# Optimization experiments

Hardware: AMD Instinct MI355X
Metric: run time of the kernel (lower is better)

The kernel has to match this reference:

```python
import jax, jax.numpy as jnp
import numpy as np
from jax import lax

B, L, D = 2, 2048, 128
H, HD = 8, 32
WIN = 3

def setup_inputs() -> dict:
    key = jax.random.key(0)
    ks = jax.random.split(key, 7)
    s = 0.05
    return {
        "x":  jax.random.normal(ks[0], (B, L, D), jnp.float32),
        "pe": jax.random.normal(ks[1], (L, D), jnp.float32) * s,
        "Wq": jax.random.normal(ks[2], (D, H * HD), jnp.float32) * s,
        "bq": jnp.zeros((H * HD,), jnp.float32),
        "Wk": jax.random.normal(ks[3], (D, H * HD), jnp.float32) * s,
        "bk": jnp.zeros((H * HD,), jnp.float32),
        "Wv": jax.random.normal(ks[4], (D, H), jnp.float32) * s,
    }

def reference(x, pe, Wq, bq, Wk, bk, Wv):
    b, l, d = x.shape
    h = Wv.shape[1]
    hd = Wq.shape[1] // h
    xp = x + pe                                   # (B,L,D)
    # split heads: Dense output columns [i*hd:(i+1)*hd] -> head i
    q = (xp @ Wq + bq).reshape(b, l, h, hd).transpose(2, 0, 1, 3)  # (H,B,L,hd)
    k = (xp @ Wk + bk).reshape(b, l, h, hd).transpose(2, 0, 1, 3)  # (H,B,L,hd)
    v = jax.nn.sigmoid(x @ Wv).transpose(2, 0, 1)                  # (H,B,L)

    attn = jnp.einsum('hbqd,hbkd->hbqk', q, k) * (float(hd) ** -0.5)
    attn = jax.nn.softmax(attn, axis=-1)          # (H,B,L,L)

    # band_part(0,-1) + diag_part(k=(0,L-1)) (RIGHT_LEFT align) + transpose + reverse(-2,-1)
    # collapses to the skew-gather: R[p, m] = attn[L-1-p-m, L-1-p] for p+m <= L-1 else 0
    p = jnp.arange(l)[:, None]                    # (L,1)
    m = jnp.arange(l)[None, :]                    # (1,L)
    ii = l - 1 - p - m                            # row index  (L,L)
    jj = jnp.broadcast_to(l - 1 - p, (l, l))      # col index  (L,L)
    valid = (ii >= 0)
    R = attn[:, :, jnp.where(valid, ii, 0), jj] * valid.astype(attn.dtype)  # (H,B,L,L)

    R = R * v[:, :, :, None]                      # gate by value, broadcast over distance axis

    # TF avg_pool excludes padding from the divisor
    sums = lax.reduce_window(R, 0.0, lax.add, (1, 1, 1, WIN), (1, 1, 1, 1), 'SAME')
    cnt = lax.reduce_window(jnp.ones((l,), R.dtype), 0.0, lax.add, (WIN,), (1,), 'SAME')
    pooled = sums / cnt                           # (H,B,L,L)

    # global mode: sum over position axis, -> (B, L_dist, H)
    out = pooled.sum(axis=2).transpose(1, 2, 0)
    return out
```

## Files before the change

kernel.cpp:

```cpp
#include <hip/hip_runtime.h>
#include <hip/hip_bf16.h>

#define LSEQ 2048
#define BB 2
#define DD 128
#define HH 8
#define HD 32

#define FPSCALE 524288.0f
#define RFPSCALE (1.0f / 524288.0f)
#define QSCALE 0.25503486f

typedef __bf16 bf8_t __attribute__((ext_vector_type(8)));
typedef __bf16 bf4_t __attribute__((ext_vector_type(4)));
typedef float f4_t __attribute__((ext_vector_type(4)));

static __device__ __forceinline__ float fexp2(float x) {
#if __has_builtin(__builtin_amdgcn_exp2f)
    return __builtin_amdgcn_exp2f(x);
#else
    float r;
    asm("v_exp_f32 %0, %1" : "=v"(r) : "v"(x));
    return r;
#endif
}

__global__ __launch_bounds__(256) void k_A(const float* __restrict__ x,
                                           const float* __restrict__ pe,
                                           const float* __restrict__ Wq,
                                           const float* __restrict__ Wk,
                                           const float* __restrict__ Wv,
                                           const float* __restrict__ bq,
                                           const float* __restrict__ bk,
                                           float* __restrict__ w,
                                           __bf16* __restrict__ Qb,
                                           __bf16* __restrict__ Kb,
                                           int* __restrict__ Si) {
    __shared__ __align__(16) char smem[34816];
    int gb = blockIdx.x;
    int tid = threadIdx.x;

    if (gb < 512) {
        __bf16* xs = (__bf16*)smem;
        __bf16* Wt = (__bf16*)(smem + 64 * 136 * 2);
        int jr = gb >> 3, y = gb & 7;
        int row0 = jr * 64;
        bool isK = y >= 4;
        int cbase = (y & 3) * 64;
        const float* W = isK ? Wk : Wq;

        #pragma unroll
        for (int i = 0; i < 8; i++) {
            int idx4 = tid + i * 256;
            int row = idx4 >> 5, col4 = idx4 & 31;
            float4 xv = ((const float4*)x)[row0 * 32 + idx4];
            float4 pv = ((const float4*)pe)[((row0 + row) & (LSEQ - 1)) * 32 + col4];
            bf4_t o = {(__bf16)(xv.x + pv.x), (__bf16)(xv.y + pv.y),
                       (__bf16)(xv.z + pv.z), (__bf16)(xv.w + pv.w)};
            *(bf4_t*)&xs[row * 136 + col4 * 4] = o;
        }
        #pragma unroll
        for (int i = 0; i < 8; i++) {
            int idx4 = tid + i * 256;
            int d = idx4 >> 4, c4 = (idx4 & 15) * 4;
            float4 wv4 = *(const float4*)(W + d * 256 + cbase + c4);
            Wt[(c4 + 0) * 136 + d] = (__bf16)wv4.x;
            Wt[(c4 + 1) * 136 + d] = (__bf16)wv4.y;
            Wt[(c4 + 2) * 136 + d] = (__bf16)wv4.z;
            Wt[(c4 + 3) * 136 + d] = (__bf16)wv4.w;
        }
        __syncthreads();

        int wid = tid >> 6, lane = tid & 63;
        int lm = lane & 15, lq = lane >> 4;
        int c0loc = wid * 16;
        f4_t acc0 = {0,0,0,0}, acc1 = {0,0,0,0}, acc2 = {0,0,0,0}, acc3 = {0,0,0,0};
        #pragma unroll
        for (int s = 0; s < 4; s++) {
            bf8_t bw = *(const bf8_t*)&Wt[(c0loc + lm) * 136 + lq * 8 + s * 32];
            bf8_t a0 = *(const bf8_t*)&xs[(0  + lm) * 136 + lq * 8 + s * 32];
            bf8_t a1 = *(const bf8_t*)&xs[(16 + lm) * 136 + lq * 8 + s * 32];
            bf8_t a2 = *(const bf8_t*)&xs[(32 + lm) * 136 + lq * 8 + s * 32];
            bf8_t a3 = *(const bf8_t*)&xs[(48 + lm) * 136 + lq * 8 + s * 32];
            acc0 = __builtin_amdgcn_mfma_f32_16x16x32_bf16(a0, bw, acc0, 0, 0, 0);
            acc1 = __builtin_amdgcn_mfma_f32_16x16x32_bf16(a1, bw, acc1, 0, 0, 0);
            acc2 = __builtin_amdgcn_mfma_f32_16x16x32_bf16(a2, bw, acc2, 0, 0, 0);
            acc3 = __builtin_amdgcn_mfma_f32_16x16x32_bf16(a3, bw, acc3, 0, 0, 0);
        }
        int c = cbase + c0loc + lm;
        float bv = (isK ? bk : bq)[c];
        float qs = isK ? 1.f : QSCALE;
        __bf16* Out = isK ? Kb : Qb;
        int h = c >> 5, hd = c & 31;
        f4_t accs[4] = {acc0, acc1, acc2, acc3};
        #pragma unroll
        for (int rs = 0; rs < 4; rs++) {
            #pragma unroll
            for (int r = 0; r < 4; r++) {
                int row = row0 + rs * 16 + lq * 4 + r;
                int b_ = row >> 11, l = row & (LSEQ - 1);
                Out[((h * BB + b_) * LSEQ + l) * HD + hd] =
                    (__bf16)((accs[rs][r] + bv) * qs);
            }
        }
    } else if (gb < 640) {
        float* xsf = (float*)smem;
        float* wvf = (float*)(smem + 32 * 132 * 4);
        int r0 = (gb - 512) * 32;
        for (int i = 0; i < 16; i++) {
            int idx = tid + i * 256;
            xsf[(idx >> 7) * 132 + (idx & 127)] = x[r0 * 128 + idx];
        }
        for (int i = 0; i < 4; i++) {
            int idx = tid + i * 256;
            wvf[idx] = Wv[idx];
        }
        __syncthreads();
        int rl = tid >> 3, h = tid & 7;
        float acc = 0.f;
        #pragma unroll 8
        for (int d = 0; d < 128; d++) acc += xsf[rl * 132 + d] * wvf[d * 8 + h];
        float sg = 1.f / (1.f + __expf(-acc));
        int r = r0 + rl;
        int b = r >> 11, l = r & (LSEQ - 1);
        w[(h * BB + b) * LSEQ + (LSEQ - 1 - l)] = sg * FPSCALE;
    } else {
        int4 z = {0, 0, 0, 0};
        ((int4*)Si)[(gb - 640) * 256 + tid] = z;
    }
}

__global__ __launch_bounds__(256) void k_F(const __bf16* __restrict__ Qb,
                                           const __bf16* __restrict__ Kb,
                                           const float* __restrict__ w,
                                           int* __restrict__ S) {
    __shared__ int Sloc[2048];
    __shared__ float dred[64];
    __shared__ float rdv_s[16];

    int hb = blockIdx.y;
    int q0 = blockIdx.x << 4;
    int tid = threadIdx.x;
    int wid = tid >> 6, lane = tid & 63;
    int lm = lane & 15, lq = lane >> 4;

    int4 z4 = {0, 0, 0, 0};
    ((int4*)Sloc)[tid] = z4;
    ((int4*)Sloc)[tid + 256] = z4;

    const __bf16* Qhb = Qb + hb * LSEQ * HD;
    const __bf16* Khb = Kb + hb * LSEQ * HD;
    bf8_t aq = *(const bf8_t*)(Qhb + (q0 + lm) * HD + lq * 8);

    float dsum[4] = {0.f, 0.f, 0.f, 0.f};
    #pragma unroll 4
    for (int s = wid; s < 128; s += 4) {
        bf8_t bk_ = *(const bf8_t*)(Khb + (s * 16 + lm) * HD + lq * 8);
        f4_t z = {0.f, 0.f, 0.f, 0.f};
        f4_t sc = __builtin_amdgcn_mfma_f32_16x16x32_bf16(aq, bk_, z, 0, 0, 0);
        #pragma unroll
        for (int r = 0; r < 4; r++) dsum[r] += fexp2(sc[r]);
    }
    #pragma unroll
    for (int r = 0; r < 4; r++) {
        float v = dsum[r];
        v += __shfl_xor(v, 1);
        v += __shfl_xor(v, 2);
        v += __shfl_xor(v, 4);
        v += __shfl_xor(v, 8);
        dsum[r] = v;
    }
    if (lm == 0) {
        #pragma unroll
        for (int r = 0; r < 4; r++) dred[wid * 16 + lq * 4 + r] = dsum[r];
    }
    __syncthreads();
    if (tid < 16) {
        float d = dred[tid] + dred[16 + tid] + dred[32 + tid] + dred[48 + tid];
        rdv_s[tid] = 1.0f / d;
    }
    __syncthreads();
    float rdv[4];
    #pragma unroll
    for (int r = 0; r < 4; r++) rdv[r] = rdv_s[lq * 4 + r];

    int nsub = 128 - (q0 >> 4);
    const float* whb = w + hb * LSEQ;
    int qrow = q0 + lq * 4;
    int qc = (nsub + 3) >> 2;
    int jlo = wid * qc;
    int jhi = jlo + qc; if (jhi > nsub) jhi = nsub;

    if (wid == 0) {
        bf8_t bk_ = *(const bf8_t*)(Khb + (q0 + lm) * HD + lq * 8);
        f4_t z = {0.f, 0.f, 0.f, 0.f};
        f4_t sc = __builtin_amdgcn_mfma_f32_16x16x32_bf16(aq, bk_, z, 0, 0, 0);
        float wv = whb[q0 + lm];
        #pragma unroll
        for (int r = 0; r < 4; r++) {
            int m = lm - lq * 4 - r;
            if (m >= 0) {
                int iv = __float2int_rn(fexp2(sc[r]) * rdv[r] * wv);
                atomicAdd(&Sloc[m], iv);
            }
        }
        jlo = 1;
    }
    #pragma unroll 2
    for (int j = jlo; j < jhi; j++) {
        int k0s = q0 + j * 16;
        bf8_t bk_ = *(const bf8_t*)(Khb + (k0s + lm) * HD + lq * 8);
        f4_t z = {0.f, 0.f, 0.f, 0.f};
        f4_t sc = __builtin_amdgcn_mfma_f32_16x16x32_bf16(aq, bk_, z, 0, 0, 0);
        float wv = whb[k0s + lm];
        int base = k0s + lm - qrow;
        #pragma unroll
        for (int r = 0; r < 4; r++) {
            int iv = __float2int_rn(fexp2(sc[r]) * rdv[r] * wv);
            atomicAdd(&Sloc[base - r], iv);
        }
    }
    __syncthreads();

    int M = LSEQ - q0;
    int* Sg = S + hb * LSEQ;
    for (int i = tid; i < M; i += 256) {
        int v = Sloc[i];
        if (v) atomicAdd(&Sg[i], v);
    }
}

__global__ __launch_bounds__(256) void k_out(const int* __restrict__ S,
                                             float* __restrict__ out) {
    int idx = blockIdx.x * 256 + threadIdx.x;
    int h = idx & 7;
    int m = (idx >> 3) & (LSEQ - 1);
    int b = idx >> 14;
    const int* Sr = S + (h * BB + b) * LSEQ;
    float s = (float)Sr[m];
    float cnt = 3.f;
    if (m > 0) s += (float)Sr[m - 1]; else cnt = 2.f;
    if (m < LSEQ - 1) s += (float)Sr[m + 1]; else cnt = 2.f;
    out[idx] = s * RFPSCALE / cnt;
}

extern "C" void kernel_launch(void* const* d_in, const int* in_sizes, int n_in,
                              void* d_out, int out_size, void* d_ws, size_t ws_size,
                              hipStream_t stream) {
    const float* x  = (const float*)d_in[0];
    const float* pe = (const float*)d_in[1];
    const float* Wq = (const float*)d_in[2];
    const float* bq = (const float*)d_in[3];
    const float* Wk = (const float*)d_in[4];
    const float* bk = (const float*)d_in[5];
    const float* Wv = (const float*)d_in[6];
    float* out = (float*)d_out;

    char* ws = (char*)d_ws;
    int*    Si  = (int*)(ws);
    float*  w   = (float*)(ws + 131072);
    __bf16* Qb  = (__bf16*)(ws + 262144);
    __bf16* Kb  = (__bf16*)(ws + 262144 + 2097152);

    k_A<<<672, 256, 0, stream>>>(x, pe, Wq, Wk, Wv, bq, bk, w, Qb, Kb, Si);
    k_F<<<dim3(128, 16), 256, 0, stream>>>(Qb, Kb, w, Si);
    k_out<<<128, 256, 0, stream>>>(Si, out);
}
```

Measured before the change: 113.9 us.

## Process two query tiles per 512-thread block in k_F, interleave key tiles across waves

Each k_F block now covers 32 query rows with 8 waves in two groups of four, one group per 16-row query tile, so the block count halves. Both groups accumulate into the same shared histogram, which means fewer zero-fill and global atomic flush passes per query row. Key tiles are now dealt to waves in round-robin order rather than in contiguous chunks, which changes load balance across waves. The separate reduction step and its barrier are dropped: each thread computes the softmax denominator reciprocals directly from shared memory. In exchange, the larger blocks and more contention on shared-memory atomics could lower occupancy.

```diff
diff --git a/kernel.cpp b/kernel.cpp
--- a/kernel.cpp
+++ b/kernel.cpp
@@ -130,31 +130,31 @@
     }
 }
 
-__global__ __launch_bounds__(256) void k_F(const __bf16* __restrict__ Qb,
+__global__ __launch_bounds__(512) void k_F(const __bf16* __restrict__ Qb,
                                            const __bf16* __restrict__ Kb,
                                            const float* __restrict__ w,
                                            int* __restrict__ S) {
     __shared__ int Sloc[2048];
-    __shared__ float dred[64];
-    __shared__ float rdv_s[16];
+    __shared__ float dred[128];
 
     int hb = blockIdx.y;
-    int q0 = blockIdx.x << 4;
+    int q0 = blockIdx.x << 5;
     int tid = threadIdx.x;
     int wid = tid >> 6, lane = tid & 63;
     int lm = lane & 15, lq = lane >> 4;
+    int g = wid >> 2, h = wid & 3;
+    int qg0 = q0 + g * 16;
 
     int4 z4 = {0, 0, 0, 0};
     ((int4*)Sloc)[tid] = z4;
-    ((int4*)Sloc)[tid + 256] = z4;
 
     const __bf16* Qhb = Qb + hb * LSEQ * HD;
     const __bf16* Khb = Kb + hb * LSEQ * HD;
-    bf8_t aq = *(const bf8_t*)(Qhb + (q0 + lm) * HD + lq * 8);
+    bf8_t aq = *(const bf8_t*)(Qhb + (qg0 + lm) * HD + lq * 8);
 
     float dsum[4] = {0.f, 0.f, 0.f, 0.f};
     #pragma unroll 4
-    for (int s = wid; s < 128; s += 4) {
+    for (int s = h; s < 128; s += 4) {
         bf8_t bk_ = *(const bf8_t*)(Khb + (s * 16 + lm) * HD + lq * 8);
         f4_t z = {0.f, 0.f, 0.f, 0.f};
         f4_t sc = __builtin_amdgcn_mfma_f32_16x16x32_bf16(aq, bk_, z, 0, 0, 0);
@@ -175,27 +175,22 @@
         for (int r = 0; r < 4; r++) dred[wid * 16 + lq * 4 + r] = dsum[r];
     }
     __syncthreads();
-    if (tid < 16) {
-        float d = dred[tid] + dred[16 + tid] + dred[32 + tid] + dred[48 + tid];
-        rdv_s[tid] = 1.0f / d;
-    }
-    __syncthreads();
     float rdv[4];
     #pragma unroll
-    for (int r = 0; r < 4; r++) rdv[r] = rdv_s[lq * 4 + r];
-
-    int nsub = 128 - (q0 >> 4);
+    for (int r = 0; r < 4; r++) {
+        int base = g * 64 + lq * 4 + r;
+        float d = dred[base] + dred[base + 16] + dred[base + 32] + dred[base + 48];
+        rdv[r] = 1.0f / d;
+    }
+
     const float* whb = w + hb * LSEQ;
-    int qrow = q0 + lq * 4;
-    int qc = (nsub + 3) >> 2;
-    int jlo = wid * qc;
-    int jhi = jlo + qc; if (jhi > nsub) jhi = nsub;
-
-    if (wid == 0) {
-        bf8_t bk_ = *(const bf8_t*)(Khb + (q0 + lm) * HD + lq * 8);
+    int qrow = qg0 + lq * 4;
+
+    if (h == 0) {
+        bf8_t bk_ = *(const bf8_t*)(Khb + (qg0 + lm) * HD + lq * 8);
         f4_t z = {0.f, 0.f, 0.f, 0.f};
         f4_t sc = __builtin_amdgcn_mfma_f32_16x16x32_bf16(aq, bk_, z, 0, 0, 0);
-        float wv = whb[q0 + lm];
+        float wv = whb[qg0 + lm];
         #pragma unroll
         for (int r = 0; r < 4; r++) {
             int m = lm - lq * 4 - r;
@@ -204,11 +199,11 @@
                 atomicAdd(&Sloc[m], iv);
             }
         }
-        jlo = 1;
-    }
+    }
+    int nfull = 127 - (qg0 >> 4);
     #pragma unroll 2
-    for (int j = jlo; j < jhi; j++) {
-        int k0s = q0 + j * 16;
+    for (int t = h; t < nfull; t += 4) {
+        int k0s = qg0 + 16 + t * 16;
         bf8_t bk_ = *(const bf8_t*)(Khb + (k0s + lm) * HD + lq * 8);
         f4_t z = {0.f, 0.f, 0.f, 0.f};
         f4_t sc = __builtin_amdgcn_mfma_f32_16x16x32_bf16(aq, bk_, z, 0, 0, 0);
@@ -224,7 +219,7 @@
 
     int M = LSEQ - q0;
     int* Sg = S + hb * LSEQ;
-    for (int i = tid; i < M; i += 256) {
+    for (int i = tid; i < M; i += 512) {
         int v = Sloc[i];
         if (v) atomicAdd(&Sg[i], v);
     }
@@ -263,6 +258,6 @@
     __bf16* Kb  = (__bf16*)(ws + 262144 + 2097152);
 
     k_A<<<672, 256, 0, stream>>>(x, pe, Wq, Wk, Wv, bq, bk, w, Qb, Kb, Si);
-    k_F<<<dim3(128, 16), 256, 0, stream>>>(Qb, Kb, w, Si);
+    k_F<<<dim3(64, 16), 512, 0, stream>>>(Qb, Kb, w, Si);
     k_out<<<128, 256, 0, stream>>>(Si, out);
 }
```

New measurement: 113.0 us. Within noise of the previous version (-0.8%).
